# Kernel optimization log

Measured on AMD Instinct MI355X. Metric: run time of the kernel, lower is better.

The kernel has to match this reference:

```python
import jax, jax.numpy as jnp
import numpy as np


def setup_inputs() -> dict:
    key = jax.random.key(0)
    k1, k2 = jax.random.split(key)
    N = 8192
    preds = jax.random.normal(k1, (N,), dtype=jnp.float32)
    targets = jax.random.normal(k2, (N,), dtype=jnp.float32)
    return {"preds": preds, "targets": targets}


def reference(preds, targets):
    n = preds.shape[0]
    # torch.std is unbiased (ddof=1)
    margin = 0.25 * jnp.std(targets, ddof=1)
    # broadcasted all-pairs differences: [N, N]
    tdiff = targets[:, None] - targets[None, :]
    pdiff = preds[:, None] - preds[None, :]
    loss = jnp.maximum(-jnp.sign(tdiff) * pdiff + margin, 0.0)
    # only pairs with i < j (strict upper triangle)
    mask = jnp.triu(jnp.ones((n, n), dtype=bool), k=1)
    num_pairs = n * (n - 1) // 2
    total = jnp.sum(jnp.where(mask, loss, 0.0))
    return total / num_pairs
```

## Files before the change

### kernel.cpp

```cpp
#include <hip/hip_runtime.h>

#define NT 256
#define SPLIT 4
#define ROWS 16

__device__ __forceinline__ float pair_loss(float tt, float pp, float tj, float pj, float margin) {
    float td = tt - tj;
    float pd = pp - pj;
    float cs = copysignf(1.0f, td);
    return fmaxf(fmaf(-cs, pd, margin), 0.0f);
}

__device__ __forceinline__ void do_j(float tj, float pj, const float* tg, const float* pg,
                                     float margin, float* av) {
    #pragma unroll
    for (int k = 0; k < ROWS; ++k) av[k] += pair_loss(tg[k], pg[k], tj, pj, margin);
}

__global__ __launch_bounds__(NT, 4)
void pair_kernel(const float* __restrict__ preds, const float* __restrict__ targets,
                 double* __restrict__ partials, int N)
{
    const int tid = threadIdx.x, lane = tid & 63, wave = tid >> 6;
    __shared__ double redd[2 * (NT / 64)];
    __shared__ float smargin;

    {
        double s = 0.0, s2 = 0.0;
        const int n4 = N >> 2;
        const float4* t4 = (const float4*)targets;
        for (int i = tid; i < n4; i += NT) {
            float4 v = t4[i];
            s  += (double)v.x + (double)v.y + (double)v.z + (double)v.w;
            s2 += (double)v.x * v.x + (double)v.y * v.y + (double)v.z * v.z + (double)v.w * v.w;
        }
        for (int i = (n4 << 2) + tid; i < N; i += NT) { float t = targets[i]; s += t; s2 += (double)t * t; }
        #pragma unroll
        for (int off = 32; off; off >>= 1) { s += __shfl_down(s, off, 64); s2 += __shfl_down(s2, off, 64); }
        if (lane == 0) { redd[wave] = s; redd[NT / 64 + wave] = s2; }
        __syncthreads();
        if (tid == 0) {
            double S = 0.0, S2 = 0.0;
            for (int w = 0; w < NT / 64; ++w) { S += redd[w]; S2 += redd[NT / 64 + w]; }
            double mean = S / (double)N;
            double var  = (S2 - (double)N * mean * mean) / (double)(N - 1);
            smargin = (float)(0.25 * sqrt(var > 0.0 ? var : 0.0));
        }
        __syncthreads();
    }
    const float margin = smargin;

    const int G = N >> 4;
    const int P = G >> 1;
    const int NB = (int)gridDim.x;
    const int sub = (int)(blockIdx.x & (SPLIT - 1));
    const int pairblk = (int)(blockIdx.x >> 2);
    const int PSTRIDE = NB >> 2;

    float av[ROWS];
    #pragma unroll
    for (int k = 0; k < ROWS; ++k) av[k] = 0.0f;
    float extra = 0.0f;

    for (int p = pairblk; p < P; p += PSTRIDE) {
        #pragma unroll
        for (int side = 0; side < 2; ++side) {
            const int gg = side ? (G - 1 - p) : p;
            const int i0 = gg << 4;
            float tg[ROWS], pg[ROWS];
            #pragma unroll
            for (int k = 0; k < ROWS; ++k) { tg[k] = targets[i0 + k]; pg[k] = preds[i0 + k]; }

            if (sub == side) {
                int ii = tid >> 4, jj = tid & 15;
                if (ii < jj) {
                    float td = tg[ii] - tg[jj], pd = pg[ii] - pg[jj];
                    float cs = (td > 0.0f) ? 1.0f : ((td < 0.0f) ? -1.0f : 0.0f);
                    extra += fmaxf(fmaf(-cs, pd, margin), 0.0f);
                }
            }

            const int lo = i0 + ROWS;
            const int len = N - lo;
            const int len4 = len >> 2;
            const float4* tj4 = (const float4*)(targets + lo);
            const float4* pj4 = (const float4*)(preds + lo);
            for (int idx = sub * NT + tid; idx < len4; idx += NT * SPLIT) {
                float4 tv = tj4[idx];
                float4 pv = pj4[idx];
                do_j(tv.x, pv.x, tg, pg, margin, av);
                do_j(tv.y, pv.y, tg, pg, margin, av);
                do_j(tv.z, pv.z, tg, pg, margin, av);
                do_j(tv.w, pv.w, tg, pg, margin, av);
            }
            for (int j = lo + (len4 << 2) + sub * NT + tid; j < N; j += NT * SPLIT) {
                do_j(targets[j], preds[j], tg, pg, margin, av);
            }
        }
    }

    if (pairblk == 0) {
        if (G & 1) {
            const int i0 = (G >> 1) << 4;
            for (int k = 0; k < ROWS && i0 + k < N; ++k) {
                const int i = i0 + k;
                for (int j = i + 1 + sub * NT + tid; j < N; j += NT * SPLIT) {
                    float td = targets[i] - targets[j], pd = preds[i] - preds[j];
                    float cs = (td > 0.0f) ? 1.0f : ((td < 0.0f) ? -1.0f : 0.0f);
                    extra += fmaxf(fmaf(-cs, pd, margin), 0.0f);
                }
            }
        }
        for (int i = G << 4; i < N; ++i) {
            for (int j = i + 1 + sub * NT + tid; j < N; j += NT * SPLIT) {
                float td = targets[i] - targets[j], pd = preds[i] - preds[j];
                float cs = (td > 0.0f) ? 1.0f : ((td < 0.0f) ? -1.0f : 0.0f);
                extra += fmaxf(fmaf(-cs, pd, margin), 0.0f);
            }
        }
    }

    double tot = (double)extra;
    #pragma unroll
    for (int k = 0; k < ROWS; ++k) tot += (double)av[k];
    #pragma unroll
    for (int off = 32; off; off >>= 1) tot += __shfl_down(tot, off, 64);
    __syncthreads();
    if (lane == 0) redd[wave] = tot;
    __syncthreads();
    if (tid == 0) {
        double bt = 0.0;
        for (int w = 0; w < NT / 64; ++w) bt += redd[w];
        partials[blockIdx.x] = bt;
    }
}

__global__ __launch_bounds__(NT)
void finalize_kernel(const double* __restrict__ partials, int nparts,
                     float* __restrict__ out, double inv_pairs)
{
    __shared__ double red[NT / 64];
    const int tid = threadIdx.x, lane = tid & 63, wave = tid >> 6;
    double s = 0.0;
    for (int i = tid; i < nparts; i += NT) s += partials[i];
    #pragma unroll
    for (int off = 32; off; off >>= 1) s += __shfl_down(s, off, 64);
    if (lane == 0) red[wave] = s;
    __syncthreads();
    if (tid == 0) {
        double t = 0.0;
        for (int w = 0; w < NT / 64; ++w) t += red[w];
        out[0] = (float)(t * inv_pairs);
    }
}

extern "C" void kernel_launch(void* const* d_in, const int* in_sizes, int n_in,
                              void* d_out, int out_size, void* d_ws, size_t ws_size,
                              hipStream_t stream) {
    const float* preds   = (const float*)d_in[0];
    const float* targets = (const float*)d_in[1];
    float* out = (float*)d_out;
    int N = in_sizes[0];

    double* partials = (double*)d_ws;
    const int G = N >> 4;
    const int P = G >> 1;

    int NB = (P > 0 ? P : 1) * SPLIT;
    if (NB > 1024) NB = 1024;
    int maxParts = (int)(ws_size / sizeof(double));
    if (NB > maxParts) NB = (maxParts / SPLIT) * SPLIT;
    if (NB < SPLIT) NB = SPLIT;

    const double inv_pairs = 2.0 / ((double)N * (double)(N - 1));
    pair_kernel<<<NB, NT, 0, stream>>>(preds, targets, partials, N);
    finalize_kernel<<<1, NT, 0, stream>>>(partials, NB, out, inv_pairs);
}
```

Before: 20.66 us.

## Fuse finalize into pair kernel via last-block atomic tree reduction

Merges the separate finalize launch into the main kernel. Each block publishes its partial sum, then bumps a two-level atomic counter (leaf groups of 32, root of 8), and the last block to arrive reduces all partials and writes the output. The grid is also reshaped to 256 blocks of 1024 threads with 8-row groups instead of split sub-blocks, trading per-thread register reuse for wider blocks. The counters are never reset, and the code relies on modulo wrap so that repeated launches stay correct, which assumes the counters start at zero and that NBLK=256 exactly matches the leaf/root arithmetic. It also drops the ws_size bound check.

Result: slower. 21.55 us (+4.3%).

```diff
diff --git a/kernel.cpp b/kernel.cpp
--- a/kernel.cpp
+++ b/kernel.cpp
@@ -1,8 +1,8 @@
 #include <hip/hip_runtime.h>
 
-#define NT 256
-#define SPLIT 4
-#define ROWS 16
+#define NT   1024
+#define NBLK 256
+#define ROWS 8
 
 __device__ __forceinline__ float pair_loss(float tt, float pp, float tj, float pj, float margin) {
     float td = tt - tj;
@@ -18,12 +18,17 @@
 }
 
 __global__ __launch_bounds__(NT, 4)
-void pair_kernel(const float* __restrict__ preds, const float* __restrict__ targets,
-                 double* __restrict__ partials, int N)
+void fused_kernel(const float* __restrict__ preds, const float* __restrict__ targets,
+                  double* __restrict__ partials,
+                  unsigned int* __restrict__ leaf,
+                  unsigned int* __restrict__ root,
+                  float* __restrict__ out, int N, double inv_pairs)
 {
     const int tid = threadIdx.x, lane = tid & 63, wave = tid >> 6;
+    const int bid = (int)blockIdx.x;
     __shared__ double redd[2 * (NT / 64)];
     __shared__ float smargin;
+    __shared__ int sflag;
 
     {
         double s = 0.0, s2 = 0.0;
@@ -50,29 +55,25 @@
     }
     const float margin = smargin;
 
-    const int G = N >> 4;
+    const int G = N >> 3;
     const int P = G >> 1;
-    const int NB = (int)gridDim.x;
-    const int sub = (int)(blockIdx.x & (SPLIT - 1));
-    const int pairblk = (int)(blockIdx.x >> 2);
-    const int PSTRIDE = NB >> 2;
 
     float av[ROWS];
     #pragma unroll
     for (int k = 0; k < ROWS; ++k) av[k] = 0.0f;
     float extra = 0.0f;
 
-    for (int p = pairblk; p < P; p += PSTRIDE) {
+    for (int p = bid; p < P; p += NBLK) {
         #pragma unroll
         for (int side = 0; side < 2; ++side) {
             const int gg = side ? (G - 1 - p) : p;
-            const int i0 = gg << 4;
+            const int i0 = gg << 3;
             float tg[ROWS], pg[ROWS];
             #pragma unroll
             for (int k = 0; k < ROWS; ++k) { tg[k] = targets[i0 + k]; pg[k] = preds[i0 + k]; }
 
-            if (sub == side) {
-                int ii = tid >> 4, jj = tid & 15;
+            if (tid < 64) {
+                int ii = tid >> 3, jj = tid & 7;
                 if (ii < jj) {
                     float td = tg[ii] - tg[jj], pd = pg[ii] - pg[jj];
                     float cs = (td > 0.0f) ? 1.0f : ((td < 0.0f) ? -1.0f : 0.0f);
@@ -85,7 +86,7 @@
             const int len4 = len >> 2;
             const float4* tj4 = (const float4*)(targets + lo);
             const float4* pj4 = (const float4*)(preds + lo);
-            for (int idx = sub * NT + tid; idx < len4; idx += NT * SPLIT) {
+            for (int idx = tid; idx < len4; idx += NT) {
                 float4 tv = tj4[idx];
                 float4 pv = pj4[idx];
                 do_j(tv.x, pv.x, tg, pg, margin, av);
@@ -93,26 +94,26 @@
                 do_j(tv.z, pv.z, tg, pg, margin, av);
                 do_j(tv.w, pv.w, tg, pg, margin, av);
             }
-            for (int j = lo + (len4 << 2) + sub * NT + tid; j < N; j += NT * SPLIT) {
+            for (int j = lo + (len4 << 2) + tid; j < N; j += NT) {
                 do_j(targets[j], preds[j], tg, pg, margin, av);
             }
         }
     }
 
-    if (pairblk == 0) {
+    if (bid == 0) {
         if (G & 1) {
-            const int i0 = (G >> 1) << 4;
+            const int i0 = (G >> 1) << 3;
             for (int k = 0; k < ROWS && i0 + k < N; ++k) {
                 const int i = i0 + k;
-                for (int j = i + 1 + sub * NT + tid; j < N; j += NT * SPLIT) {
+                for (int j = i + 1 + tid; j < N; j += NT) {
                     float td = targets[i] - targets[j], pd = preds[i] - preds[j];
                     float cs = (td > 0.0f) ? 1.0f : ((td < 0.0f) ? -1.0f : 0.0f);
                     extra += fmaxf(fmaf(-cs, pd, margin), 0.0f);
                 }
             }
         }
-        for (int i = G << 4; i < N; ++i) {
-            for (int j = i + 1 + sub * NT + tid; j < N; j += NT * SPLIT) {
+        for (int i = G << 3; i < N; ++i) {
+            for (int j = i + 1 + tid; j < N; j += NT) {
                 float td = targets[i] - targets[j], pd = preds[i] - preds[j];
                 float cs = (td > 0.0f) ? 1.0f : ((td < 0.0f) ? -1.0f : 0.0f);
                 extra += fmaxf(fmaf(-cs, pd, margin), 0.0f);
@@ -128,29 +129,29 @@
     __syncthreads();
     if (lane == 0) redd[wave] = tot;
     __syncthreads();
+
     if (tid == 0) {
         double bt = 0.0;
         for (int w = 0; w < NT / 64; ++w) bt += redd[w];
-        partials[blockIdx.x] = bt;
+        __hip_atomic_store(&partials[bid], bt, __ATOMIC_RELAXED, __HIP_MEMORY_SCOPE_AGENT);
+        const unsigned g = (unsigned)bid >> 5;
+        unsigned lv = __hip_atomic_fetch_add(&leaf[g], 1u, __ATOMIC_ACQ_REL, __HIP_MEMORY_SCOPE_AGENT);
+        int f = 0;
+        if ((lv & 31u) == 31u) {
+            unsigned rv = __hip_atomic_fetch_add(root, 1u, __ATOMIC_ACQ_REL, __HIP_MEMORY_SCOPE_AGENT);
+            if ((rv & 7u) == 7u) f = 1;
+        }
+        sflag = f;
     }
-}
+    __syncthreads();
 
-__global__ __launch_bounds__(NT)
-void finalize_kernel(const double* __restrict__ partials, int nparts,
-                     float* __restrict__ out, double inv_pairs)
-{
-    __shared__ double red[NT / 64];
-    const int tid = threadIdx.x, lane = tid & 63, wave = tid >> 6;
-    double s = 0.0;
-    for (int i = tid; i < nparts; i += NT) s += partials[i];
-    #pragma unroll
-    for (int off = 32; off; off >>= 1) s += __shfl_down(s, off, 64);
-    if (lane == 0) red[wave] = s;
-    __syncthreads();
-    if (tid == 0) {
-        double t = 0.0;
-        for (int w = 0; w < NT / 64; ++w) t += red[w];
-        out[0] = (float)(t * inv_pairs);
+    if (sflag != 0 && tid < 64) {
+        double s = 0.0;
+        for (int i = lane; i < NBLK; i += 64)
+            s += __hip_atomic_load(&partials[i], __ATOMIC_RELAXED, __HIP_MEMORY_SCOPE_AGENT);
+        #pragma unroll
+        for (int off = 32; off; off >>= 1) s += __shfl_down(s, off, 64);
+        if (lane == 0) out[0] = (float)(s * inv_pairs);
     }
 }
 
@@ -162,17 +163,10 @@
     float* out = (float*)d_out;
     int N = in_sizes[0];
 
-    double* partials = (double*)d_ws;
-    const int G = N >> 4;
-    const int P = G >> 1;
-
-    int NB = (P > 0 ? P : 1) * SPLIT;
-    if (NB > 1024) NB = 1024;
-    int maxParts = (int)(ws_size / sizeof(double));
-    if (NB > maxParts) NB = (maxParts / SPLIT) * SPLIT;
-    if (NB < SPLIT) NB = SPLIT;
+    double*       partials = (double*)d_ws;
+    unsigned int* leaf     = (unsigned int*)((char*)d_ws + NBLK * sizeof(double));
+    unsigned int* root     = leaf + 8;
 
     const double inv_pairs = 2.0 / ((double)N * (double)(N - 1));
-    pair_kernel<<<NB, NT, 0, stream>>>(preds, targets, partials, N);
-    finalize_kernel<<<1, NT, 0, stream>>>(partials, NB, out, inv_pairs);
+    fused_kernel<<<NBLK, NT, 0, stream>>>(preds, targets, partials, leaf, root, out, N, inv_pairs);
 }
```

## Hoist margin reduction into separate kernel and shrink row tile to 8

Applied to the files above, without the earlier changes.

Moves the std/margin reduction out of every pair block into a single 1024-thread kernel whose result pair blocks read from workspace. This removes the redundant full-array scan each of the 1024 blocks did before its pair work. It also halves ROWS to 8 and SPLIT to 2, changing per-thread reuse and the work split across blocks. The cost is an extra kernel launch on the critical path and less register reuse per loaded j element.

Measured after the change: 20.69 us. No clear change (+0.2%).

```diff
diff --git a/kernel.cpp b/kernel.cpp
--- a/kernel.cpp
+++ b/kernel.cpp
@@ -1,8 +1,8 @@
 #include <hip/hip_runtime.h>
 
-#define NT 256
-#define SPLIT 4
-#define ROWS 16
+#define NT    256
+#define SPLIT 2
+#define ROWS  8
 
 __device__ __forceinline__ float pair_loss(float tt, float pp, float tj, float pj, float margin) {
     float td = tt - tj;
@@ -17,45 +17,50 @@
     for (int k = 0; k < ROWS; ++k) av[k] += pair_loss(tg[k], pg[k], tj, pj, margin);
 }
 
+__global__ __launch_bounds__(1024)
+void margin_kernel(const float* __restrict__ targets, int N, float* __restrict__ margin_out)
+{
+    const int tid = threadIdx.x, lane = tid & 63, wave = tid >> 6;
+    __shared__ double redd[2 * 16];
+    double s = 0.0, s2 = 0.0;
+    const int n4 = N >> 2;
+    const float4* t4 = (const float4*)targets;
+    for (int i = tid; i < n4; i += 1024) {
+        float4 v = t4[i];
+        s  += (double)v.x + (double)v.y + (double)v.z + (double)v.w;
+        s2 += (double)v.x * v.x + (double)v.y * v.y + (double)v.z * v.z + (double)v.w * v.w;
+    }
+    for (int i = (n4 << 2) + tid; i < N; i += 1024) { float t = targets[i]; s += t; s2 += (double)t * t; }
+    #pragma unroll
+    for (int off = 32; off; off >>= 1) { s += __shfl_down(s, off, 64); s2 += __shfl_down(s2, off, 64); }
+    if (lane == 0) { redd[wave] = s; redd[16 + wave] = s2; }
+    __syncthreads();
+    if (tid == 0) {
+        double S = 0.0, S2 = 0.0;
+        const int nw = (int)(blockDim.x >> 6);
+        for (int w = 0; w < nw; ++w) { S += redd[w]; S2 += redd[16 + w]; }
+        double mean = S / (double)N;
+        double var  = (S2 - (double)N * mean * mean) / (double)(N - 1);
+        margin_out[0] = (float)(0.25 * sqrt(var > 0.0 ? var : 0.0));
+    }
+}
+
 __global__ __launch_bounds__(NT, 4)
 void pair_kernel(const float* __restrict__ preds, const float* __restrict__ targets,
+                 const float* __restrict__ margin_p,
                  double* __restrict__ partials, int N)
 {
     const int tid = threadIdx.x, lane = tid & 63, wave = tid >> 6;
-    __shared__ double redd[2 * (NT / 64)];
-    __shared__ float smargin;
+    __shared__ double redd[NT / 64];
 
-    {
-        double s = 0.0, s2 = 0.0;
-        const int n4 = N >> 2;
-        const float4* t4 = (const float4*)targets;
-        for (int i = tid; i < n4; i += NT) {
-            float4 v = t4[i];
-            s  += (double)v.x + (double)v.y + (double)v.z + (double)v.w;
-            s2 += (double)v.x * v.x + (double)v.y * v.y + (double)v.z * v.z + (double)v.w * v.w;
-        }
-        for (int i = (n4 << 2) + tid; i < N; i += NT) { float t = targets[i]; s += t; s2 += (double)t * t; }
-        #pragma unroll
-        for (int off = 32; off; off >>= 1) { s += __shfl_down(s, off, 64); s2 += __shfl_down(s2, off, 64); }
-        if (lane == 0) { redd[wave] = s; redd[NT / 64 + wave] = s2; }
-        __syncthreads();
-        if (tid == 0) {
-            double S = 0.0, S2 = 0.0;
-            for (int w = 0; w < NT / 64; ++w) { S += redd[w]; S2 += redd[NT / 64 + w]; }
-            double mean = S / (double)N;
-            double var  = (S2 - (double)N * mean * mean) / (double)(N - 1);
-            smargin = (float)(0.25 * sqrt(var > 0.0 ? var : 0.0));
-        }
-        __syncthreads();
-    }
-    const float margin = smargin;
+    const float margin = margin_p[0];
 
-    const int G = N >> 4;
+    const int G = N >> 3;
     const int P = G >> 1;
     const int NB = (int)gridDim.x;
     const int sub = (int)(blockIdx.x & (SPLIT - 1));
-    const int pairblk = (int)(blockIdx.x >> 2);
-    const int PSTRIDE = NB >> 2;
+    const int pairblk = (int)(blockIdx.x >> 1);
+    const int PSTRIDE = NB >> 1;
 
     float av[ROWS];
     #pragma unroll
@@ -66,13 +71,13 @@
         #pragma unroll
         for (int side = 0; side < 2; ++side) {
             const int gg = side ? (G - 1 - p) : p;
-            const int i0 = gg << 4;
+            const int i0 = gg << 3;
             float tg[ROWS], pg[ROWS];
             #pragma unroll
             for (int k = 0; k < ROWS; ++k) { tg[k] = targets[i0 + k]; pg[k] = preds[i0 + k]; }
 
-            if (sub == side) {
-                int ii = tid >> 4, jj = tid & 15;
+            if (sub == side && tid < 64) {
+                int ii = tid >> 3, jj = tid & 7;
                 if (ii < jj) {
                     float td = tg[ii] - tg[jj], pd = pg[ii] - pg[jj];
                     float cs = (td > 0.0f) ? 1.0f : ((td < 0.0f) ? -1.0f : 0.0f);
@@ -101,7 +106,7 @@
 
     if (pairblk == 0) {
         if (G & 1) {
-            const int i0 = (G >> 1) << 4;
+            const int i0 = (G >> 1) << 3;
             for (int k = 0; k < ROWS && i0 + k < N; ++k) {
                 const int i = i0 + k;
                 for (int j = i + 1 + sub * NT + tid; j < N; j += NT * SPLIT) {
@@ -111,7 +116,7 @@
                 }
             }
         }
-        for (int i = G << 4; i < N; ++i) {
+        for (int i = G << 3; i < N; ++i) {
             for (int j = i + 1 + sub * NT + tid; j < N; j += NT * SPLIT) {
                 float td = targets[i] - targets[j], pd = preds[i] - preds[j];
                 float cs = (td > 0.0f) ? 1.0f : ((td < 0.0f) ? -1.0f : 0.0f);
@@ -125,7 +130,6 @@
     for (int k = 0; k < ROWS; ++k) tot += (double)av[k];
     #pragma unroll
     for (int off = 32; off; off >>= 1) tot += __shfl_down(tot, off, 64);
-    __syncthreads();
     if (lane == 0) redd[wave] = tot;
     __syncthreads();
     if (tid == 0) {
@@ -163,16 +167,15 @@
     int N = in_sizes[0];
 
     double* partials = (double*)d_ws;
-    const int G = N >> 4;
+    float*  marg     = (float*)((char*)d_ws + 1024 * 8);
+
+    const int G = N >> 3;
     const int P = G >> 1;
-
     int NB = (P > 0 ? P : 1) * SPLIT;
     if (NB > 1024) NB = 1024;
-    int maxParts = (int)(ws_size / sizeof(double));
-    if (NB > maxParts) NB = (maxParts / SPLIT) * SPLIT;
-    if (NB < SPLIT) NB = SPLIT;
 
     const double inv_pairs = 2.0 / ((double)N * (double)(N - 1));
-    pair_kernel<<<NB, NT, 0, stream>>>(preds, targets, partials, N);
+    margin_kernel<<<1, 1024, 0, stream>>>(targets, N, marg);
+    pair_kernel<<<NB, NT, 0, stream>>>(preds, targets, marg, partials, N);
     finalize_kernel<<<1, NT, 0, stream>>>(partials, NB, out, inv_pairs);
 }
```
